# Kernel tuning notes

Hardware: AMD Instinct MI355X
Metric: run time of the kernel (lower is better)

## Reference

```python
import jax, jax.numpy as jnp
import numpy as np
from jax import lax

A = 20            # len(ANCHOR_RATIOS)=4 * len(ANCHOR_SCALES)=5 in neural-motifs config
TGT = 6           # anchor_target_dim
DIM = 512
IN_DIM = 1024
B, H, W = 16, 37, 37


def setup_inputs() -> dict:
    key = jax.random.key(0)
    k1, k2, k3, k4, k5 = jax.random.split(key, 5)
    fmap = jax.random.normal(k1, (B, IN_DIM, H, W), dtype=jnp.float32)
    # conv weights in OIHW, fan-in scaled init
    W1 = jax.random.normal(k2, (DIM, IN_DIM, 3, 3), dtype=jnp.float32) / np.sqrt(IN_DIM * 9)
    b1 = jnp.zeros((DIM,), dtype=jnp.float32)
    W2 = jax.random.normal(k3, (TGT * A, DIM, 1, 1), dtype=jnp.float32) / np.sqrt(DIM)
    b2 = jnp.zeros((TGT * A,), dtype=jnp.float32)
    return {"fmap": fmap, "W1": W1, "b1": b1, "W2": W2, "b2": b2}


def reference(fmap, W1, b1, W2, b2):
    dn = ("NCHW", "OIHW", "NCHW")
    # 3x3 conv, padding=1
    x = lax.conv_general_dilated(fmap, W1, window_strides=(1, 1), padding="SAME",
                                 dimension_numbers=dn) + b1[None, :, None, None]
    # ReLU6
    x = jnp.clip(x, 0.0, 6.0)
    # 1x1 conv -> [B, 6*A, H, W]
    x = lax.conv_general_dilated(x, W2, window_strides=(1, 1), padding="VALID",
                                 dimension_numbers=dn) + b2[None, :, None, None]
    # _reshape_channels: [B, C, H, W] -> [B, H, W, C], then split C -> (A, 6)
    b, c, h, w = x.shape
    x = jnp.transpose(x, (0, 2, 3, 1))
    return x.reshape(b, h, w, A, TGT)
```

## Files before the change

### kernel.cpp

```cpp
#include <hip/hip_runtime.h>
#include <stdint.h>

#define HW   1369
#define QW   39
#define QP   1616
#define QT   1536
#define CIN  1024
#define CMID 512
#define KTOT 9216
#define NTIL 144
#define SLOT 28672

typedef float  f32x4  __attribute__((ext_vector_type(4)));
typedef __bf16 bf16x8 __attribute__((ext_vector_type(8)));

__device__ __forceinline__ uint16_t f2bf(float f) {
  uint32_t u = __float_as_uint(f);
  u += 0x7fffu + ((u >> 16) & 1u);
  return (uint16_t)(u >> 16);
}

__device__ __forceinline__ void gll16(const void* g, void* l) {
  const __attribute__((address_space(1))) uint32_t* ga =
      (const __attribute__((address_space(1))) uint32_t*)(uintptr_t)g;
  __attribute__((address_space(3))) uint32_t* la =
      (__attribute__((address_space(3))) uint32_t*)(uint32_t)(uintptr_t)l;
  __builtin_amdgcn_global_load_lds(ga, la, 16, 0, 0);
}

__global__ void k_pad_transpose(const float* __restrict__ fmap, uint16_t* __restrict__ Xp) {
  __shared__ float t[32][33];
  const int b = blockIdx.z;
  const int c0 = blockIdx.y * 32;
  const int p0 = blockIdx.x * 32;
  const int tx = threadIdx.x, ty = threadIdx.y;
  const float* src = fmap + ((size_t)b * CIN + c0) * HW + p0;
#pragma unroll
  for (int i = 0; i < 4; ++i) {
    int cc = ty + i * 8;
    t[cc][tx] = (p0 + tx < HW) ? src[(size_t)cc * HW + tx] : 0.f;
  }
  __syncthreads();
#pragma unroll
  for (int i = 0; i < 4; ++i) {
    int pl = ty + i * 8;
    int p = p0 + pl;
    if (p < HW) {
      int h = p / 37, w = p - h * 37;
      int q = (h + 1) * QW + (w + 1);
      Xp[((size_t)b * QP + q) * CIN + c0 + tx] = f2bf(t[tx][pl]);
    }
  }
}

__global__ void k_pack_w1(const float* __restrict__ W1, uint16_t* __restrict__ Apk) {
  int idx = blockIdx.x * 256 + threadIdx.x;
  if (idx >= 512 * KTOT) return;
  int o = idx / KTOT, k = idx - o * KTOT;
  int r = k >> 10, c = k & 1023;
  Apk[idx] = f2bf(W1[((size_t)o * CIN + c) * 9 + r]);
}

__global__ void k_pack_w2(const float* __restrict__ W2, uint16_t* __restrict__ W2p) {
  int idx = blockIdx.x * 256 + threadIdx.x;
  int j = idx >> 9, o = idx & 511;
  W2p[idx] = (j < 120) ? f2bf(W2[j * 512 + o]) : (uint16_t)0;
}

__global__ __launch_bounds__(512, 1) void k_conv1(
    const uint16_t* __restrict__ Xp, const uint16_t* __restrict__ Apk,
    const float* __restrict__ b1, uint16_t* __restrict__ x1) {
  __shared__ __align__(16) uint16_t lds[2 * SLOT];

  const int tid  = threadIdx.x;
  const int wid  = tid >> 6, lane = tid & 63;
  const int lrow = lane & 15, lq = lane >> 4;
  const int wm   = wid >> 2,  wn = wid & 3;

  const int bid = blockIdx.x;
  const int g   = (bid & 7) * 32 + (bid >> 3);
  const int mt  = g >> 1, nt = g & 1;
  const int batch = mt >> 3, qb = (mt & 7) * 192;
  const int o0 = nt * 256;
  const uint16_t* Xb = Xp + (size_t)batch * QP * CIN;

  const int xorb    = (lrow & 7) << 4;
  const int col_el0 = ((lq * 16) ^ xorb) >> 1;
  const int col_el1 = col_el0 ^ 32;

  const int scol = ((tid & 7) ^ ((tid >> 3) & 7)) * 8;
  const int srow = tid >> 3;

  f32x4 acc[6][4] = {};

#define STAGE(u) do {                                                                 \
    if ((u) < NTIL) {                                                                 \
      const int cb_  = (u) / 9;                                                       \
      const int tap_ = (u) - cb_ * 9;                                                 \
      const int off_ = (tap_ / 3) * QW + tap_ % 3;                                    \
      const int c0_  = cb_ << 6;                                                      \
      uint16_t* sl = lds + ((u) & 1) * SLOT;                                          \
      _Pragma("unroll")                                                               \
      for (int j = 0; j < 3; ++j)                                                     \
        gll16(Xb + (size_t)(qb + off_ + j * 64 + srow) * CIN + c0_ + scol,            \
              sl + j * 4096 + wid * 512);                                             \
      _Pragma("unroll")                                                               \
      for (int j = 0; j < 4; ++j)                                                     \
        gll16(Apk + (size_t)(o0 + j * 64 + srow) * KTOT + (tap_ << 10) + c0_ + scol,  \
              sl + 12288 + j * 4096 + wid * 512);                                     \
    }                                                                                 \
  } while (0)

#define PHASE(MH, KK, RDBV) do {                                                      \
    const int ce = (KK) ? col_el1 : col_el0;                                          \
    bf16x8 av[3];                                                                     \
    if (RDBV) {                                                                       \
      _Pragma("unroll")                                                               \
      for (int n = 0; n < 4; ++n)                                                     \
        bv[n] = *(const bf16x8*)(Bs + (wn * 64 + n * 16 + lrow) * 64 + ce);           \
    }                                                                                 \
    _Pragma("unroll")                                                                 \
    for (int m = 0; m < 3; ++m)                                                       \
      av[m] = *(const bf16x8*)(As + (wm * 96 + (MH) * 48 + m * 16 + lrow) * 64 + ce); \
    asm volatile("s_barrier" ::: "memory");                                           \
    asm volatile("s_waitcnt lgkmcnt(0)" ::: "memory");                                \
    __builtin_amdgcn_sched_barrier(0);                                                \
    __builtin_amdgcn_s_setprio(1);                                                    \
    _Pragma("unroll")                                                                 \
    for (int m = 0; m < 3; ++m)                                                       \
      _Pragma("unroll")                                                               \
      for (int n = 0; n < 4; ++n)                                                     \
        acc[(MH) * 3 + m][n] = __builtin_amdgcn_mfma_f32_16x16x32_bf16(               \
            av[m], bv[n], acc[(MH) * 3 + m][n], 0, 0, 0);                             \
    __builtin_amdgcn_s_setprio(0);                                                    \
    asm volatile("s_barrier" ::: "memory");                                           \
    __builtin_amdgcn_sched_barrier(0);                                                \
  } while (0)

  STAGE(0);

  for (int t = 0; t < NTIL; ++t) {
    const uint16_t* As = lds + (t & 1) * SLOT;
    const uint16_t* Bs = As + 12288;
    asm volatile("s_waitcnt vmcnt(0)" ::: "memory");
    asm volatile("s_barrier" ::: "memory");
    __builtin_amdgcn_sched_barrier(0);
    STAGE(t + 1);
    bf16x8 bv[4];
    PHASE(0, 0, 1);
    PHASE(1, 0, 0);
    PHASE(0, 1, 1);
    PHASE(1, 1, 0);
  }

  const int qr = lq * 4;
#pragma unroll
  for (int n = 0; n < 4; ++n) {
    const int o = o0 + wn * 64 + n * 16 + lrow;
    const float bias = b1[o];
#pragma unroll
    for (int m = 0; m < 6; ++m) {
#pragma unroll
      for (int v = 0; v < 4; ++v) {
        const int q = qb + wm * 96 + m * 16 + qr + v;
        float x = acc[m][n][v] + bias;
        x = fminf(fmaxf(x, 0.f), 6.f);
        x1[((size_t)batch * QT + q) * CMID + o] = f2bf(x);
      }
    }
  }
#undef PHASE
#undef STAGE
}

__global__ __launch_bounds__(256, 2) void k_conv2(
    const uint16_t* __restrict__ x1, const uint16_t* __restrict__ W2p,
    const float* __restrict__ b2, float* __restrict__ out) {
  __shared__ __align__(16) uint16_t lA[128 * 64];
  __shared__ __align__(16) uint16_t lB[128 * 64];
  const int tid = threadIdx.x;
  const int wid = tid >> 6, lane = tid & 63;
  const int b = blockIdx.z, q0 = blockIdx.x * 128;
  const uint16_t* Ab = x1 + (size_t)b * QT * CMID;
  const int wm = wid >> 1, wn = wid & 1;
  const int lrow = lane & 15, lk = (lane >> 4) * 8;
  f32x4 acc[4][4] = {};

  for (int kt = 0; kt < 8; ++kt) {
    const int c0 = kt << 6;
#pragma unroll
    for (int i = 0; i < 4; ++i) {
      int wb = i * 256 + wid * 64;
      int chunk = wb + lane;
      int row = chunk >> 3, ch = chunk & 7;
      gll16(Ab + (size_t)(q0 + row) * CMID + c0 + ch * 8, lA + wb * 8);
      gll16(W2p + (size_t)row * CMID + c0 + ch * 8, lB + wb * 8);
    }
    __syncthreads();
#pragma unroll
    for (int kk = 0; kk < 2; ++kk) {
      bf16x8 av[4], bv[4];
#pragma unroll
      for (int mi = 0; mi < 4; ++mi)
        av[mi] = *(const bf16x8*)(lA + (wm * 64 + mi * 16 + lrow) * 64 + kk * 32 + lk);
#pragma unroll
      for (int ni = 0; ni < 4; ++ni)
        bv[ni] = *(const bf16x8*)(lB + (wn * 64 + ni * 16 + lrow) * 64 + kk * 32 + lk);
#pragma unroll
      for (int mi = 0; mi < 4; ++mi)
#pragma unroll
        for (int ni = 0; ni < 4; ++ni)
          acc[mi][ni] = __builtin_amdgcn_mfma_f32_16x16x32_bf16(av[mi], bv[ni], acc[mi][ni], 0, 0, 0);
    }
    __syncthreads();
  }

  const int qr = (lane >> 4) * 4;
#pragma unroll
  for (int ni = 0; ni < 4; ++ni) {
    int j = wn * 64 + ni * 16 + lrow;
    if (j < 120) {
      float bias = b2[j];
#pragma unroll
      for (int mi = 0; mi < 4; ++mi) {
#pragma unroll
        for (int v = 0; v < 4; ++v) {
          int q = q0 + wm * 64 + mi * 16 + qr + v;
          int h = q / QW, w = q - h * QW;
          if (h < 37 && w < 37) {
            out[((size_t)b * HW + h * 37 + w) * 120 + j] = acc[mi][ni][v] + bias;
          }
        }
      }
    }
  }
}

extern "C" void kernel_launch(void* const* d_in, const int* in_sizes, int n_in,
                              void* d_out, int out_size, void* d_ws, size_t ws_size,
                              hipStream_t stream) {
  const float* fmap = (const float*)d_in[0];
  const float* W1   = (const float*)d_in[1];
  const float* b1   = (const float*)d_in[2];
  const float* W2   = (const float*)d_in[3];
  const float* b2   = (const float*)d_in[4];
  float* out = (float*)d_out;

  uint8_t* ws = (uint8_t*)d_ws;
  const size_t XP_BYTES  = (size_t)16 * QP * CIN * 2;
  const size_t W1P_BYTES = (size_t)512 * KTOT * 2;
  const size_t W2P_BYTES = (size_t)128 * 512 * 2;
  uint16_t* Xp  = (uint16_t*)ws;
  uint16_t* Apk = (uint16_t*)(ws + XP_BYTES);
  uint16_t* W2p = (uint16_t*)(ws + XP_BYTES + W1P_BYTES);
  uint16_t* x1  = (uint16_t*)(ws + XP_BYTES + W1P_BYTES + W2P_BYTES);

  hipMemsetAsync(Xp, 0, XP_BYTES, stream);
  k_pad_transpose<<<dim3(43, 32, 16), dim3(32, 8), 0, stream>>>(fmap, Xp);
  k_pack_w1<<<dim3((512 * KTOT + 255) / 256), dim3(256), 0, stream>>>(W1, Apk);
  k_pack_w2<<<dim3(256), dim3(256), 0, stream>>>(W2, W2p);
  k_conv1<<<dim3(256), dim3(512), 0, stream>>>(Xp, Apk, b1, x1);
  k_conv2<<<dim3(12, 1, 16), dim3(256), 0, stream>>>(x1, W2p, b2, out);
}
```

Before: 283.6 us.

## Triple-buffer activation tiles and drop per-phase barriers in conv1 main loop

The conv1 GEMM loop now gives the activation (A) tiles three LDS slots and the weight (B) tiles two. A is prefetched two iterations ahead and B one ahead, and a partial `vmcnt(3)` wait lets the newest A load stay in flight. The four barrier-separated MFMA phases per tile are replaced by one block that reads all A/B fragments and then issues both K-halves of MFMAs, removing eight barriers per iteration. This aims to hide more global-load latency and cut synchronisation stalls. In exchange it uses more LDS (about 136 KB) and more vector registers for the fragments held at once.

Result: faster. 263.3 us (-7.2%).

```diff
diff --git a/kernel.cpp b/kernel.cpp
--- a/kernel.cpp
+++ b/kernel.cpp
@@ -9,7 +9,9 @@
 #define CMID 512
 #define KTOT 9216
 #define NTIL 144
-#define SLOT 28672
+#define ASL  12288
+#define BBASE 36864
+#define BSL  16384
 
 typedef float  f32x4  __attribute__((ext_vector_type(4)));
 typedef __bf16 bf16x8 __attribute__((ext_vector_type(8)));
@@ -70,7 +72,7 @@
 __global__ __launch_bounds__(512, 1) void k_conv1(
     const uint16_t* __restrict__ Xp, const uint16_t* __restrict__ Apk,
     const float* __restrict__ b1, uint16_t* __restrict__ x1) {
-  __shared__ __align__(16) uint16_t lds[2 * SLOT];
+  __shared__ __align__(16) uint16_t lds[BBASE + 2 * BSL];
 
   const int tid  = threadIdx.x;
   const int wid  = tid >> 6, lane = tid & 63;
@@ -93,64 +95,72 @@
 
   f32x4 acc[6][4] = {};
 
-#define STAGE(u) do {                                                                 \
+#define STAGEA(u) do {                                                                \
     if ((u) < NTIL) {                                                                 \
       const int cb_  = (u) / 9;                                                       \
       const int tap_ = (u) - cb_ * 9;                                                 \
       const int off_ = (tap_ / 3) * QW + tap_ % 3;                                    \
       const int c0_  = cb_ << 6;                                                      \
-      uint16_t* sl = lds + ((u) & 1) * SLOT;                                          \
+      uint16_t* sl = lds + ((u) % 3) * ASL;                                           \
       _Pragma("unroll")                                                               \
       for (int j = 0; j < 3; ++j)                                                     \
         gll16(Xb + (size_t)(qb + off_ + j * 64 + srow) * CIN + c0_ + scol,            \
               sl + j * 4096 + wid * 512);                                             \
+    }                                                                                 \
+  } while (0)
+
+#define STAGEB(u) do {                                                                \
+    if ((u) < NTIL) {                                                                 \
+      const int cb_  = (u) / 9;                                                       \
+      const int tap_ = (u) - cb_ * 9;                                                 \
+      const int c0_  = cb_ << 6;                                                      \
+      uint16_t* sl = lds + BBASE + ((u) & 1) * BSL;                                   \
       _Pragma("unroll")                                                               \
       for (int j = 0; j < 4; ++j)                                                     \
         gll16(Apk + (size_t)(o0 + j * 64 + srow) * KTOT + (tap_ << 10) + c0_ + scol,  \
-              sl + 12288 + j * 4096 + wid * 512);                                     \
+              sl + j * 4096 + wid * 512);                                             \
     }                                                                                 \
   } while (0)
 
-#define PHASE(MH, KK, RDBV) do {                                                      \
-    const int ce = (KK) ? col_el1 : col_el0;                                          \
-    bf16x8 av[3];                                                                     \
-    if (RDBV) {                                                                       \
-      _Pragma("unroll")                                                               \
-      for (int n = 0; n < 4; ++n)                                                     \
-        bv[n] = *(const bf16x8*)(Bs + (wn * 64 + n * 16 + lrow) * 64 + ce);           \
-    }                                                                                 \
-    _Pragma("unroll")                                                                 \
-    for (int m = 0; m < 3; ++m)                                                       \
-      av[m] = *(const bf16x8*)(As + (wm * 96 + (MH) * 48 + m * 16 + lrow) * 64 + ce); \
-    asm volatile("s_barrier" ::: "memory");                                           \
-    asm volatile("s_waitcnt lgkmcnt(0)" ::: "memory");                                \
-    __builtin_amdgcn_sched_barrier(0);                                                \
-    __builtin_amdgcn_s_setprio(1);                                                    \
-    _Pragma("unroll")                                                                 \
-    for (int m = 0; m < 3; ++m)                                                       \
-      _Pragma("unroll")                                                               \
-      for (int n = 0; n < 4; ++n)                                                     \
-        acc[(MH) * 3 + m][n] = __builtin_amdgcn_mfma_f32_16x16x32_bf16(               \
-            av[m], bv[n], acc[(MH) * 3 + m][n], 0, 0, 0);                             \
-    __builtin_amdgcn_s_setprio(0);                                                    \
-    asm volatile("s_barrier" ::: "memory");                                           \
-    __builtin_amdgcn_sched_barrier(0);                                                \
-  } while (0)
-
-  STAGE(0);
+  STAGEB(0);
+  STAGEA(0);
+  STAGEA(1);
 
   for (int t = 0; t < NTIL; ++t) {
-    const uint16_t* As = lds + (t & 1) * SLOT;
-    const uint16_t* Bs = As + 12288;
-    asm volatile("s_waitcnt vmcnt(0)" ::: "memory");
+    const uint16_t* As = lds + (t % 3) * ASL;
+    const uint16_t* Bs = lds + BBASE + (t & 1) * BSL;
+    if (t == NTIL - 1) asm volatile("s_waitcnt vmcnt(0)" ::: "memory");
+    else               asm volatile("s_waitcnt vmcnt(3)" ::: "memory");
     asm volatile("s_barrier" ::: "memory");
     __builtin_amdgcn_sched_barrier(0);
-    STAGE(t + 1);
-    bf16x8 bv[4];
-    PHASE(0, 0, 1);
-    PHASE(1, 0, 0);
-    PHASE(0, 1, 1);
-    PHASE(1, 1, 0);
+    STAGEB(t + 1);
+    STAGEA(t + 2);
+
+    bf16x8 av0[6], av1[6], bv0[4], bv1[4];
+#pragma unroll
+    for (int n = 0; n < 4; ++n) {
+      const uint16_t* br = Bs + (wn * 64 + n * 16 + lrow) * 64;
+      bv0[n] = *(const bf16x8*)(br + col_el0);
+      bv1[n] = *(const bf16x8*)(br + col_el1);
+    }
+#pragma unroll
+    for (int m = 0; m < 6; ++m) {
+      const uint16_t* ar = As + (wm * 96 + m * 16 + lrow) * 64;
+      av0[m] = *(const bf16x8*)(ar + col_el0);
+      av1[m] = *(const bf16x8*)(ar + col_el1);
+    }
+    __builtin_amdgcn_s_setprio(1);
+#pragma unroll
+    for (int m = 0; m < 6; ++m)
+#pragma unroll
+      for (int n = 0; n < 4; ++n)
+        acc[m][n] = __builtin_amdgcn_mfma_f32_16x16x32_bf16(av0[m], bv0[n], acc[m][n], 0, 0, 0);
+#pragma unroll
+    for (int m = 0; m < 6; ++m)
+#pragma unroll
+      for (int n = 0; n < 4; ++n)
+        acc[m][n] = __builtin_amdgcn_mfma_f32_16x16x32_bf16(av1[m], bv1[n], acc[m][n], 0, 0, 0);
+    __builtin_amdgcn_s_setprio(0);
   }
 
   const int qr = lq * 4;
@@ -169,8 +179,8 @@
       }
     }
   }
-#undef PHASE
-#undef STAGE
+#undef STAGEB
+#undef STAGEA
 }
 
 __global__ __launch_bounds__(256, 2) void k_conv2(
```
